# Kernel optimization log

Hardware: AMD Instinct MI355X
Metric: run time of the kernel (lower is better)

Reference implementation:

```python
import jax, jax.numpy as jnp
import numpy as np

B, LQ, LK, D = 16, 1024, 4096, 256
SQRT_SCALE_INV = 0.25          # D ** -0.25, so scale = 1/sqrt(D)
HALF_BW = 128 // 2             # stripe_bandwdith // 2
NEG_INF = float('-inf')


def setup_inputs() -> dict:
    key = jax.random.key(0)
    k1, k2, k3, k4 = jax.random.split(key, 4)
    query = jax.random.normal(k1, (B, LQ, D), jnp.float32)
    key_t = jax.random.normal(k2, (B, LK, D), jnp.float32)
    value = jax.random.normal(k3, (B, LK, D), jnp.float32)
    # key lengths in [LK//2, LK]; masked_fill in torch requires max == LK
    key_lengths = jax.random.randint(k4, (B,), LK // 2, LK + 1).astype(jnp.int32)
    key_lengths = key_lengths.at[0].set(LK)
    query_lengths = jnp.full((B,), LQ, dtype=jnp.int32)  # full so no all-masked rows
    mask = jnp.arange(LK)[None, :] < key_lengths[:, None]  # [B, LK] bool, True = valid
    return {"query": query, "key": key_t, "value": value, "mask": mask,
            "query_lengths": query_lengths, "key_lengths": key_lengths}


def _stripe_mask(query_lengths, key_lengths, Lq, Lk):
    # band around line y = x * (key_len / query_len), per sample
    gx = jnp.arange(Lq, dtype=jnp.float32)[None, :, None]   # [1,Lq,1]
    gy = jnp.arange(Lk, dtype=jnp.float32)[None, None, :]   # [1,1,Lk]
    slope = (key_lengths.astype(jnp.float32) /
             query_lengths.astype(jnp.float32))[:, None, None]  # [B,1,1]
    center = gx * slope
    return (gy >= center - HALF_BW) & (gy <= center + HALF_BW)  # [B,Lq,Lk] bool


def reference(query, key, value, mask, query_lengths, key_lengths):
    # scores = (q * s) @ (k * s)^T  ==  (q @ k^T) * s^2
    scores = jnp.einsum('bqd,bkd->bqk', query, key) * (SQRT_SCALE_INV * SQRT_SCALE_INV)
    stripe = _stripe_mask(query_lengths, key_lengths, query.shape[1], key.shape[1])
    full_mask = mask[:, None, :] & stripe                    # padding AND stripe
    scores = jnp.where(full_mask, scores.astype(jnp.float32), NEG_INF)
    weight = jax.nn.softmax(scores, axis=-1).astype(query.dtype)
    # module applies no dropout (p=0) and returns (attn_weight, value)
    return (weight, value)
```

## Files before the change

### kernel.cpp

```cpp
#include <hip/hip_runtime.h>
#include <math.h>

constexpr int B_  = 16;
constexpr int LQ_ = 1024;
constexpr int LK_ = 4096;
constexpr int D_  = 256;
constexpr float HALF_BW_F = 64.0f;
constexpr float SCALE = 0.0625f;

typedef float fx4 __attribute__((ext_vector_type(4)));

constexpr int NB_PAD = 168;
constexpr int ROWS_PER_BLK = 16;
constexpr int NUNIT = (B_ * LQ_) / ROWS_PER_BLK;
constexpr int NXCD = 8;
constexpr int UNIT_PER_XCD = NUNIT / NXCD;

template <int CTRL>
__device__ __forceinline__ float dpp_add(float v) {
    int x = __builtin_amdgcn_update_dpp(0, __float_as_int(v), CTRL, 0xF, 0xF, true);
    return v + __int_as_float(x);
}

__device__ __forceinline__ float grp16_max(float v) {
    #pragma unroll
    for (int off = 8; off > 0; off >>= 1)
        v = fmaxf(v, __shfl_xor(v, off, 64));
    return v;
}
__device__ __forceinline__ float grp16_sum(float v) {
    #pragma unroll
    for (int off = 8; off > 0; off >>= 1)
        v += __shfl_xor(v, off, 64);
    return v;
}

__global__ __launch_bounds__(256, 2) void stripe_attn_kernel(
    const float* __restrict__ Q, const float* __restrict__ K,
    const float* __restrict__ V,
    const int* __restrict__ qlen, const int* __restrict__ klen,
    float* __restrict__ Wout, float* __restrict__ Vout)
{
    const int Bid  = blockIdx.x;
    const int xcd  = Bid & 7;
    const int type = (Bid >> 3) & 1;
    const int rb   = xcd * UNIT_PER_XCD + (Bid >> 4);
    const int tid  = threadIdx.x;
    const int lane = tid & 63;
    const int wave = tid >> 6;
    const int row0 = rb * ROWS_PER_BLK + wave * 4;
    const int b    = row0 >> 10;
    const int qi0  = row0 & (LQ_ - 1);

    __shared__ float s_sc[4][4 * NB_PAD];

    const int   key_len = klen[b];
    const float slope   = (float)key_len / (float)qlen[b];

    int k_lo[4], k_hi[4];
    #pragma unroll
    for (int r = 0; r < 4; ++r) {
        const float center = (float)(qi0 + r) * slope;
        int lo = (int)ceilf(center - HALF_BW_F); if (lo < 0) lo = 0;
        int hi = (int)floorf(center + HALF_BW_F); if (hi > key_len - 1) hi = key_len - 1;
        k_lo[r] = lo; k_hi[r] = hi;
    }

    if (type == 1) {
        const float* vs = V    + (size_t)row0 * 1024;
        float*       vd = Vout + (size_t)row0 * 1024;
        #pragma unroll
        for (int it = 0; it < 16; ++it) {
            const int o = (it * 64 + lane) * 4;
            fx4 t = __builtin_nontemporal_load((const fx4*)(vs + o));
            __builtin_nontemporal_store(t, (fx4*)(vd + o));
        }
        const fx4 z4 = {0.f, 0.f, 0.f, 0.f};
        #pragma unroll
        for (int r = 0; r < 4; ++r) {
            const int s_lo = k_lo[r] >> 8, s_hi = k_hi[r] >> 8;
            float* base = Wout + (size_t)(row0 + r) * LK_;
            #pragma unroll
            for (int j = 0; j < 16; ++j) {
                if (j < s_lo || j > s_hi)
                    __builtin_nontemporal_store(z4, (fx4*)(base + (j * 64 + lane) * 4));
            }
        }
        return;
    }

    const int g   = lane >> 4;
    const int l   = lane & 15;
    const int lo0 = k_lo[0], hi3 = k_hi[3];

    const float* qbase = Q + ((size_t)b * LQ_ + qi0) * D_;
    float4 q0[4], q1[4], q2[4], q3[4];
    #pragma unroll
    for (int m = 0; m < 4; ++m) {
        q0[m] = *(const float4*)(qbase + 0 * D_ + l * 16 + m * 4);
        q1[m] = *(const float4*)(qbase + 1 * D_ + l * 16 + m * 4);
        q2[m] = *(const float4*)(qbase + 2 * D_ + l * 16 + m * 4);
        q3[m] = *(const float4*)(qbase + 3 * D_ + l * 16 + m * 4);
    }

    const float* kbase = K + (size_t)b * LK_ * D_;
    float* sw = s_sc[wave];
    #pragma unroll 2
    for (int kk0 = lo0; kk0 <= hi3; kk0 += 4) {
        const int key  = kk0 + g;
        const int keyc = (key <= hi3) ? key : hi3;
        const float* kp = kbase + (size_t)keyc * D_ + l * 16;
        float4 kf[4];
        #pragma unroll
        for (int m = 0; m < 4; ++m)
            kf[m] = *(const float4*)(kp + m * 4);
        float a0 = 0.f, a1 = 0.f, a2 = 0.f, a3 = 0.f;
        #pragma unroll
        for (int m = 0; m < 4; ++m) {
            a0 += q0[m].x*kf[m].x + q0[m].y*kf[m].y + q0[m].z*kf[m].z + q0[m].w*kf[m].w;
            a1 += q1[m].x*kf[m].x + q1[m].y*kf[m].y + q1[m].z*kf[m].z + q1[m].w*kf[m].w;
            a2 += q2[m].x*kf[m].x + q2[m].y*kf[m].y + q2[m].z*kf[m].z + q2[m].w*kf[m].w;
            a3 += q3[m].x*kf[m].x + q3[m].y*kf[m].y + q3[m].z*kf[m].z + q3[m].w*kf[m].w;
        }
        a0 = dpp_add<0x118>(a0); a0 = dpp_add<0x114>(a0);
        a0 = dpp_add<0x112>(a0); a0 = dpp_add<0x111>(a0);
        a1 = dpp_add<0x118>(a1); a1 = dpp_add<0x114>(a1);
        a1 = dpp_add<0x112>(a1); a1 = dpp_add<0x111>(a1);
        a2 = dpp_add<0x118>(a2); a2 = dpp_add<0x114>(a2);
        a2 = dpp_add<0x112>(a2); a2 = dpp_add<0x111>(a2);
        a3 = dpp_add<0x118>(a3); a3 = dpp_add<0x114>(a3);
        a3 = dpp_add<0x112>(a3); a3 = dpp_add<0x111>(a3);
        if (l == 15) {
            if (key >= k_lo[0] && key <= k_hi[0]) sw[0*NB_PAD + key - k_lo[0]] = a0 * SCALE;
            if (key >= k_lo[1] && key <= k_hi[1]) sw[1*NB_PAD + key - k_lo[1]] = a1 * SCALE;
            if (key >= k_lo[2] && key <= k_hi[2]) sw[2*NB_PAD + key - k_lo[2]] = a2 * SCALE;
            if (key >= k_lo[3] && key <= k_hi[3]) sw[3*NB_PAD + key - k_lo[3]] = a3 * SCALE;
        }
    }

    const float center_g = (float)(qi0 + g) * slope;
    int klo_g = (int)ceilf(center_g - HALF_BW_F); if (klo_g < 0) klo_g = 0;
    int khi_g = (int)floorf(center_g + HALF_BW_F); if (khi_g > key_len - 1) khi_g = key_len - 1;
    const int nb_g = khi_g - klo_g + 1;
    float* sg = sw + g * NB_PAD;

    float vj[9];
    #pragma unroll
    for (int j = 0; j < 9; ++j) {
        const int idx = l + j * 16;
        vj[j] = (idx < nb_g) ? sg[idx] : -INFINITY;
    }
    float mx = vj[0];
    #pragma unroll
    for (int j = 1; j < 9; ++j) mx = fmaxf(mx, vj[j]);
    mx = grp16_max(mx);

    float ej[9], ssum = 0.f;
    #pragma unroll
    for (int j = 0; j < 9; ++j) { ej[j] = __expf(vj[j] - mx); ssum += ej[j]; }
    ssum = grp16_sum(ssum);
    const float inv = 1.0f / ssum;
    #pragma unroll
    for (int j = 0; j < 9; ++j)
        sg[l + j * 16] = ej[j] * inv;

    #pragma unroll
    for (int r = 0; r < 4; ++r) {
        const int klo = k_lo[r], khi = k_hi[r];
        const int s_lo = klo >> 8, s_hi = khi >> 8;
        float* base = Wout + (size_t)(row0 + r) * LK_;
        const float* sr = sw + r * NB_PAD;
        for (int j = s_lo; j <= s_hi; ++j) {
            const int c0 = (j * 64 + lane) * 4;
            float w[4] = {0.f, 0.f, 0.f, 0.f};
            if (c0 + 3 >= klo && c0 <= khi) {
                #pragma unroll
                for (int i = 0; i < 4; ++i) {
                    const int c = c0 + i;
                    if (c >= klo && c <= khi) w[i] = sr[c - klo];
                }
            }
            fx4 w4; w4.x = w[0]; w4.y = w[1]; w4.z = w[2]; w4.w = w[3];
            __builtin_nontemporal_store(w4, (fx4*)(base + c0));
        }
    }
}

extern "C" void kernel_launch(void* const* d_in, const int* in_sizes, int n_in,
                              void* d_out, int out_size, void* d_ws, size_t ws_size,
                              hipStream_t stream) {
    const float* Q    = (const float*)d_in[0];
    const float* K    = (const float*)d_in[1];
    const float* V    = (const float*)d_in[2];
    const int*   qlen = (const int*)d_in[4];
    const int*   klen = (const int*)d_in[5];

    float* Wout = (float*)d_out;
    const size_t W_ELEMS = (size_t)B_ * LQ_ * LK_;
    float* Vout = Wout + W_ELEMS;

    stripe_attn_kernel<<<dim3(2 * NUNIT), dim3(256), 0, stream>>>(
        Q, K, V, qlen, klen, Wout, Vout);
}
```

Before: 99.97 us.

## Compute banded QK^T scores with bf16 MFMA over 16-row wave tiles

Replaces the scalar FP32 dot-product loop with DPP reductions by bf16 MFMA 16x16x32 instructions. Each wave now handles 16 query rows and their 192-wide key window, with softmax done directly on the accumulator registers. Blocks now cover 64 rows instead of 16, so there are fewer blocks and each does more of the copy and zero-fill work. Converting Q and K to bf16 lowers score precision, which may push the softmax weights past tolerance, and the 12 accumulator tiles raise register pressure.

```diff
diff --git a/kernel.cpp b/kernel.cpp
--- a/kernel.cpp
+++ b/kernel.cpp
@@ -8,20 +8,30 @@
 constexpr float HALF_BW_F = 64.0f;
 constexpr float SCALE = 0.0625f;
 
-typedef float fx4 __attribute__((ext_vector_type(4)));
-
-constexpr int NB_PAD = 168;
-constexpr int ROWS_PER_BLK = 16;
+typedef float  fx4    __attribute__((ext_vector_type(4)));
+typedef short  bf16x8 __attribute__((ext_vector_type(8)));
+typedef float  f32x4v __attribute__((ext_vector_type(4)));
+
+constexpr int ROWS_PER_WAVE = 16;
+constexpr int ROWS_PER_BLK  = 64;
 constexpr int NUNIT = (B_ * LQ_) / ROWS_PER_BLK;
-constexpr int NXCD = 8;
+constexpr int NXCD  = 8;
 constexpr int UNIT_PER_XCD = NUNIT / NXCD;
-
-template <int CTRL>
-__device__ __forceinline__ float dpp_add(float v) {
-    int x = __builtin_amdgcn_update_dpp(0, __float_as_int(v), CTRL, 0xF, 0xF, true);
-    return v + __int_as_float(x);
-}
-
+constexpr int KSPAN = 192;
+constexpr int NT    = 12;
+
+__device__ __forceinline__ unsigned short f2bf(float f) {
+    unsigned int u = __float_as_uint(f);
+    return (unsigned short)((u + 0x7FFFu + ((u >> 16) & 1u)) >> 16);
+}
+__device__ __forceinline__ bf16x8 pack8(float4 a, float4 b) {
+    bf16x8 r;
+    r[0] = (short)f2bf(a.x); r[1] = (short)f2bf(a.y);
+    r[2] = (short)f2bf(a.z); r[3] = (short)f2bf(a.w);
+    r[4] = (short)f2bf(b.x); r[5] = (short)f2bf(b.y);
+    r[6] = (short)f2bf(b.z); r[7] = (short)f2bf(b.w);
+    return r;
+}
 __device__ __forceinline__ float grp16_max(float v) {
     #pragma unroll
     for (int off = 8; off > 0; off >>= 1)
@@ -44,41 +54,34 @@
     const int Bid  = blockIdx.x;
     const int xcd  = Bid & 7;
     const int type = (Bid >> 3) & 1;
-    const int rb   = xcd * UNIT_PER_XCD + (Bid >> 4);
+    const int slot = Bid >> 4;
+    const int cu_u = xcd * UNIT_PER_XCD + slot;
     const int tid  = threadIdx.x;
     const int lane = tid & 63;
     const int wave = tid >> 6;
-    const int row0 = rb * ROWS_PER_BLK + wave * 4;
+    const int row0 = cu_u * ROWS_PER_BLK + wave * ROWS_PER_WAVE;
     const int b    = row0 >> 10;
     const int qi0  = row0 & (LQ_ - 1);
 
-    __shared__ float s_sc[4][4 * NB_PAD];
-
     const int   key_len = klen[b];
     const float slope   = (float)key_len / (float)qlen[b];
-
-    int k_lo[4], k_hi[4];
-    #pragma unroll
-    for (int r = 0; r < 4; ++r) {
-        const float center = (float)(qi0 + r) * slope;
-        int lo = (int)ceilf(center - HALF_BW_F); if (lo < 0) lo = 0;
-        int hi = (int)floorf(center + HALF_BW_F); if (hi > key_len - 1) hi = key_len - 1;
-        k_lo[r] = lo; k_hi[r] = hi;
-    }
 
     if (type == 1) {
         const float* vs = V    + (size_t)row0 * 1024;
         float*       vd = Vout + (size_t)row0 * 1024;
         #pragma unroll
-        for (int it = 0; it < 16; ++it) {
+        for (int it = 0; it < 64; ++it) {
             const int o = (it * 64 + lane) * 4;
             fx4 t = __builtin_nontemporal_load((const fx4*)(vs + o));
             __builtin_nontemporal_store(t, (fx4*)(vd + o));
         }
         const fx4 z4 = {0.f, 0.f, 0.f, 0.f};
         #pragma unroll
-        for (int r = 0; r < 4; ++r) {
-            const int s_lo = k_lo[r] >> 8, s_hi = k_hi[r] >> 8;
+        for (int r = 0; r < 16; ++r) {
+            const float center = (float)(qi0 + r) * slope;
+            int lo = (int)ceilf(center - HALF_BW_F); if (lo < 0) lo = 0;
+            int hi = (int)floorf(center + HALF_BW_F); if (hi > key_len - 1) hi = key_len - 1;
+            const int s_lo = lo >> 8, s_hi = hi >> 8;
             float* base = Wout + (size_t)(row0 + r) * LK_;
             #pragma unroll
             for (int j = 0; j < 16; ++j) {
@@ -89,87 +92,88 @@
         return;
     }
 
-    const int g   = lane >> 4;
-    const int l   = lane & 15;
-    const int lo0 = k_lo[0], hi3 = k_hi[3];
-
-    const float* qbase = Q + ((size_t)b * LQ_ + qi0) * D_;
-    float4 q0[4], q1[4], q2[4], q3[4];
-    #pragma unroll
-    for (int m = 0; m < 4; ++m) {
-        q0[m] = *(const float4*)(qbase + 0 * D_ + l * 16 + m * 4);
-        q1[m] = *(const float4*)(qbase + 1 * D_ + l * 16 + m * 4);
-        q2[m] = *(const float4*)(qbase + 2 * D_ + l * 16 + m * 4);
-        q3[m] = *(const float4*)(qbase + 3 * D_ + l * 16 + m * 4);
-    }
-
-    const float* kbase = K + (size_t)b * LK_ * D_;
-    float* sw = s_sc[wave];
-    #pragma unroll 2
-    for (int kk0 = lo0; kk0 <= hi3; kk0 += 4) {
-        const int key  = kk0 + g;
-        const int keyc = (key <= hi3) ? key : hi3;
-        const float* kp = kbase + (size_t)keyc * D_ + l * 16;
-        float4 kf[4];
-        #pragma unroll
-        for (int m = 0; m < 4; ++m)
-            kf[m] = *(const float4*)(kp + m * 4);
-        float a0 = 0.f, a1 = 0.f, a2 = 0.f, a3 = 0.f;
-        #pragma unroll
-        for (int m = 0; m < 4; ++m) {
-            a0 += q0[m].x*kf[m].x + q0[m].y*kf[m].y + q0[m].z*kf[m].z + q0[m].w*kf[m].w;
-            a1 += q1[m].x*kf[m].x + q1[m].y*kf[m].y + q1[m].z*kf[m].z + q1[m].w*kf[m].w;
-            a2 += q2[m].x*kf[m].x + q2[m].y*kf[m].y + q2[m].z*kf[m].z + q2[m].w*kf[m].w;
-            a3 += q3[m].x*kf[m].x + q3[m].y*kf[m].y + q3[m].z*kf[m].z + q3[m].w*kf[m].w;
-        }
-        a0 = dpp_add<0x118>(a0); a0 = dpp_add<0x114>(a0);
-        a0 = dpp_add<0x112>(a0); a0 = dpp_add<0x111>(a0);
-        a1 = dpp_add<0x118>(a1); a1 = dpp_add<0x114>(a1);
-        a1 = dpp_add<0x112>(a1); a1 = dpp_add<0x111>(a1);
-        a2 = dpp_add<0x118>(a2); a2 = dpp_add<0x114>(a2);
-        a2 = dpp_add<0x112>(a2); a2 = dpp_add<0x111>(a2);
-        a3 = dpp_add<0x118>(a3); a3 = dpp_add<0x114>(a3);
-        a3 = dpp_add<0x112>(a3); a3 = dpp_add<0x111>(a3);
-        if (l == 15) {
-            if (key >= k_lo[0] && key <= k_hi[0]) sw[0*NB_PAD + key - k_lo[0]] = a0 * SCALE;
-            if (key >= k_lo[1] && key <= k_hi[1]) sw[1*NB_PAD + key - k_lo[1]] = a1 * SCALE;
-            if (key >= k_lo[2] && key <= k_hi[2]) sw[2*NB_PAD + key - k_lo[2]] = a2 * SCALE;
-            if (key >= k_lo[3] && key <= k_hi[3]) sw[3*NB_PAD + key - k_lo[3]] = a3 * SCALE;
-        }
-    }
-
-    const float center_g = (float)(qi0 + g) * slope;
-    int klo_g = (int)ceilf(center_g - HALF_BW_F); if (klo_g < 0) klo_g = 0;
-    int khi_g = (int)floorf(center_g + HALF_BW_F); if (khi_g > key_len - 1) khi_g = key_len - 1;
-    const int nb_g = khi_g - klo_g + 1;
-    float* sg = sw + g * NB_PAD;
-
-    float vj[9];
-    #pragma unroll
-    for (int j = 0; j < 9; ++j) {
-        const int idx = l + j * 16;
-        vj[j] = (idx < nb_g) ? sg[idx] : -INFINITY;
-    }
-    float mx = vj[0];
-    #pragma unroll
-    for (int j = 1; j < 9; ++j) mx = fmaxf(mx, vj[j]);
-    mx = grp16_max(mx);
-
-    float ej[9], ssum = 0.f;
-    #pragma unroll
-    for (int j = 0; j < 9; ++j) { ej[j] = __expf(vj[j] - mx); ssum += ej[j]; }
-    ssum = grp16_sum(ssum);
-    const float inv = 1.0f / ssum;
-    #pragma unroll
-    for (int j = 0; j < 9; ++j)
-        sg[l + j * 16] = ej[j] * inv;
+    __shared__ float s_sc[4][ROWS_PER_WAVE][KSPAN];
+
+    int lo_w = (int)ceilf((float)qi0 * slope - HALF_BW_F);
+    if (lo_w < 0) lo_w = 0;
+    int hi_w = (int)floorf((float)(qi0 + 15) * slope + HALF_BW_F);
+    if (hi_w > key_len - 1) hi_w = key_len - 1;
+    const int nt = (hi_w - lo_w) / 16 + 1;
+
+    const int col = lane & 15;
+    const int kg  = lane >> 4;
+
+    const float* qb = Q + ((size_t)b * LQ_ + qi0 + col) * D_ + kg * 8;
+    bf16x8 qf[8];
+    #pragma unroll
+    for (int kc = 0; kc < 8; ++kc) {
+        const float4 u = *(const float4*)(qb + kc * 32);
+        const float4 v = *(const float4*)(qb + kc * 32 + 4);
+        qf[kc] = pack8(u, v);
+    }
+
+    const float* kb = K + (size_t)b * LK_ * D_ + kg * 8;
+    f32x4v acc[NT];
+    #pragma unroll
+    for (int t = 0; t < NT; ++t) acc[t] = (f32x4v){0.f, 0.f, 0.f, 0.f};
+
+    #pragma unroll
+    for (int t = 0; t < NT; ++t) {
+        if (t < nt) {
+            const int key  = lo_w + t * 16 + col;
+            const int keyc = (key <= hi_w) ? key : hi_w;
+            const float* kp = kb + (size_t)keyc * D_;
+            float4 u[8], w[8];
+            #pragma unroll
+            for (int kc = 0; kc < 8; ++kc) {
+                u[kc] = *(const float4*)(kp + kc * 32);
+                w[kc] = *(const float4*)(kp + kc * 32 + 4);
+            }
+            #pragma unroll
+            for (int kc = 0; kc < 8; ++kc) {
+                const bf16x8 kf = pack8(u[kc], w[kc]);
+                acc[t] = __builtin_amdgcn_mfma_f32_16x16x32_bf16(qf[kc], kf, acc[t], 0, 0, 0);
+            }
+        }
+    }
 
     #pragma unroll
     for (int r = 0; r < 4; ++r) {
-        const int klo = k_lo[r], khi = k_hi[r];
+        const int rg = kg * 4 + r;
+        const float center = (float)(qi0 + rg) * slope;
+        int klo = (int)ceilf(center - HALF_BW_F); if (klo < 0) klo = 0;
+        int khi = (int)floorf(center + HALF_BW_F); if (khi > key_len - 1) khi = key_len - 1;
+
+        float v[NT];
+        #pragma unroll
+        for (int t = 0; t < NT; ++t) {
+            const int key = lo_w + t * 16 + col;
+            v[t] = (t < nt && key >= klo && key <= khi) ? acc[t][r] * SCALE : -INFINITY;
+        }
+        float mx = v[0];
+        #pragma unroll
+        for (int t = 1; t < NT; ++t) mx = fmaxf(mx, v[t]);
+        mx = grp16_max(mx);
+
+        float e[NT], ssum = 0.f;
+        #pragma unroll
+        for (int t = 0; t < NT; ++t) { e[t] = __expf(v[t] - mx); ssum += e[t]; }
+        ssum = grp16_sum(ssum);
+        const float inv = 1.0f / ssum;
+
+        #pragma unroll
+        for (int t = 0; t < NT; ++t)
+            if (t < nt) s_sc[wave][rg][t * 16 + col] = e[t] * inv;
+    }
+
+    #pragma unroll
+    for (int r = 0; r < 16; ++r) {
+        const float center = (float)(qi0 + r) * slope;
+        int klo = (int)ceilf(center - HALF_BW_F); if (klo < 0) klo = 0;
+        int khi = (int)floorf(center + HALF_BW_F); if (khi > key_len - 1) khi = key_len - 1;
         const int s_lo = klo >> 8, s_hi = khi >> 8;
         float* base = Wout + (size_t)(row0 + r) * LK_;
-        const float* sr = sw + r * NB_PAD;
+        const float* sr = &s_sc[wave][r][0];
         for (int j = s_lo; j <= s_hi; ++j) {
             const int c0 = (j * 64 + lane) * 4;
             float w[4] = {0.f, 0.f, 0.f, 0.f};
@@ -177,7 +181,7 @@
                 #pragma unroll
                 for (int i = 0; i < 4; ++i) {
                     const int c = c0 + i;
-                    if (c >= klo && c <= khi) w[i] = sr[c - klo];
+                    if (c >= klo && c <= khi) w[i] = sr[c - lo_w];
                 }
             }
             fx4 w4; w4.x = w[0]; w4.y = w[1]; w4.z = w[2]; w4.w = w[3];
```

Measured after the change: 102.6 us. 2.6% more time.
